# Optimization experiments

Measured on AMD Instinct MI355X. Metric: run time of the kernel, lower is better.

The kernel has to match this reference:

```python
import jax, jax.numpy as jnp
import numpy as np

DIM = 64
HEADS = 4

def setup_inputs() -> dict:
    key = jax.random.key(0)
    ks = jax.random.split(key, 8)
    b, c, h, w = 2, DIM, 64, 64
    x = jax.random.normal(ks[0], (b, c, h, w), dtype=jnp.float32)
    illu_feat = jax.random.normal(ks[1], (b, c, h, w), dtype=jnp.float32)
    s = 0.05
    qkv_w = jax.random.normal(ks[2], (3 * c, c), dtype=jnp.float32) * s
    qkv_b = jax.random.normal(ks[3], (3 * c,), dtype=jnp.float32) * s
    illu_w = jax.random.normal(ks[4], (c, c), dtype=jnp.float32) * s
    illu_b = jax.random.normal(ks[5], (c,), dtype=jnp.float32) * s
    proj_w = jax.random.normal(ks[6], (c, c), dtype=jnp.float32) * s
    proj_b = jax.random.normal(ks[7], (c,), dtype=jnp.float32) * s
    return {"x": x, "illu_feat": illu_feat, "qkv_w": qkv_w, "qkv_b": qkv_b,
            "illu_w": illu_w, "illu_b": illu_b, "proj_w": proj_w, "proj_b": proj_b}

def reference(x, illu_feat, qkv_w, qkv_b, illu_w, illu_b, proj_w, proj_b):
    b, c, h, w = x.shape
    heads = HEADS
    d = c // heads
    scale = float(d) ** -0.5
    hw = h * w
    # 1x1 convs are per-pixel matmuls over the channel dim
    xt = x.reshape(b, c, hw).transpose(0, 2, 1)            # [b, hw, c]
    qkv = xt @ qkv_w.T + qkv_b                              # [b, hw, 3c]
    # channel layout of qkv conv output is (three, heads, d)
    qkv = qkv.reshape(b, hw, 3, heads, d).transpose(2, 0, 3, 1, 4)  # [3, b, heads, hw, d]
    q, k, v = qkv[0], qkv[1], qkv[2]
    it = illu_feat.reshape(b, c, hw).transpose(0, 2, 1) @ illu_w.T + illu_b  # [b, hw, c]
    illu = it.reshape(b, hw, heads, d).transpose(0, 2, 1, 3)                 # [b, heads, hw, d]
    k = k + illu
    attn = jax.nn.softmax(jnp.einsum('bhnd,bhmd->bhnm', q, k) * scale, axis=-1)
    out = jnp.einsum('bhnm,bhmd->bhnd', attn, v)            # [b, heads, hw, d]
    out = out.transpose(0, 2, 1, 3).reshape(b, hw, c)       # channels = (heads, d)
    y = out @ proj_w.T + proj_b                             # [b, hw, c]
    return y.transpose(0, 2, 1).reshape(b, c, h, w)
```

## Files before the change

kernel.cpp:

```cpp
#include <hip/hip_runtime.h>
#include <hip/hip_bf16.h>
#include <math.h>

#define HW   4096
#define NC   64
#define NB   2
#define NHD  4
#define DH   16
#define NBH  (NB*NHD)

typedef __attribute__((ext_vector_type(4))) float f32x4;
typedef __attribute__((ext_vector_type(8))) short bf16x8;
typedef __attribute__((ext_vector_type(2))) unsigned int uint2v;

#define QSCALE 0.36067376022224087f

static __device__ __forceinline__ unsigned short bf16_bits(float f) {
    union { __hip_bfloat16 h; unsigned short u; } cv;
    cv.h = __float2bfloat16(f);
    return cv.u;
}
static __device__ __forceinline__ float bits_to_f(unsigned short b) {
    return __uint_as_float(((unsigned int)b) << 16);
}
static __device__ __forceinline__ unsigned int cvt_pk_bf16(float lo, float hi) {
    unsigned int r;
    asm("v_cvt_pk_bf16_f32 %0, %1, %2" : "=v"(r) : "v"(lo), "v"(hi));
    return r;
}

__global__ __launch_bounds__(256) void wprep_kernel(
    const float* __restrict__ qkv_w, const float* __restrict__ qkv_b,
    const float* __restrict__ illu_w, const float* __restrict__ illu_b,
    const float* __restrict__ proj_w,
    ushort* __restrict__ Wt, float* __restrict__ Bias, ushort* __restrict__ Wp)
{
    int idx = blockIdx.x * 256 + threadIdx.x;
    if (idx < 49152) {
        int k8 = idx & 15;
        int n  = (idx >> 4) & 15;
        int hl = (idx >> 8) & 1;
        int ct = (idx >> 9) & 7;
        int ot = idx >> 12;
        int c   = ct*16 + k8;
        int out = ot*16 + n;
        float w;
        if (ot < 4)       w = (c < 64) ? qkv_w[out*64 + c] * QSCALE : 0.f;
        else if (ot < 8)  w = (c < 64) ? qkv_w[out*64 + c]
                                       : illu_w[(out-64)*64 + (c-64)];
        else              w = (c < 64) ? qkv_w[out*64 + c] : 0.f;
        unsigned short hb = bf16_bits(w);
        Wt[idx] = (hl == 0) ? hb : bf16_bits(w - bits_to_f(hb));
    } else if (idx < 49344) {
        int out = idx - 49152;
        float bv = (out < 64)  ? qkv_b[out] * QSCALE
                 : (out < 128) ? qkv_b[out] + illu_b[out-64]
                 :               qkv_b[out];
        Bias[out] = bv;
    } else if (idx < 49344 + 8192) {
        int local = idx - 49344;
        int k8 = local & 15;
        int n  = (local >> 4) & 15;
        int hl = (local >> 8) & 1;
        int ct = (local >> 9) & 3;
        int ot = local >> 11;
        float w = proj_w[(ot*16 + n)*64 + ct*16 + k8];
        unsigned short hb = bf16_bits(w);
        Wp[local] = (hl == 0) ? hb : bf16_bits(w - bits_to_f(hb));
    }
}

__global__ __launch_bounds__(256) void qkv_kernel(
    const float* __restrict__ x, const float* __restrict__ illu,
    const ushort* __restrict__ Wt, const float* __restrict__ Bias,
    ushort* __restrict__ Qx, ushort* __restrict__ Kx, ushort* __restrict__ Vt)
{
    __shared__ alignas(16) float  xf[128*20];
    __shared__ alignas(16) ushort frag[8*16*32];

    int blk = blockIdx.x;
    int b   = blk & 1;
    int px0 = (blk >> 1) * 16;
    int tid = threadIdx.x;
    int w   = tid >> 6;
    int lane = tid & 63;
    int g   = lane >> 4;
    int n   = lane & 15;

    #pragma unroll
    for (int rep = 0; rep < 2; ++rep) {
        int id  = tid + rep*256;
        int row = id >> 2, seg = id & 3;
        const float* src = (row < 64) ? x    + (size_t)(b*NC + row)*HW
                                      : illu + (size_t)(b*NC + row - 64)*HW;
        float4 v = *(const float4*)(src + px0 + seg*4);
        *(float4*)(xf + row*20 + seg*4) = v;
    }
    __syncthreads();

    if (tid < 128) {
        int ct = tid >> 4, px = tid & 15;
        int swz = (px & 3) ^ ((px >> 2) & 3);
        union { ushort us[8]; bf16x8 v; } g0, g1, g2, g3;
        #pragma unroll
        for (int i = 0; i < 8; ++i) {
            float v  = xf[(ct*16 + i)*20 + px];
            unsigned short hb = bf16_bits(v);
            g0.us[i] = hb;
            g2.us[i] = bf16_bits(v - bits_to_f(hb));
            float v2 = xf[(ct*16 + 8 + i)*20 + px];
            unsigned short hb2 = bf16_bits(v2);
            g1.us[i] = hb2;
            g3.us[i] = bf16_bits(v2 - bits_to_f(hb2));
        }
        ushort* fb = frag + (ct*16 + px)*32;
        *(bf16x8*)(fb + ((0 ^ swz)*8)) = g0.v;
        *(bf16x8*)(fb + ((1 ^ swz)*8)) = g1.v;
        *(bf16x8*)(fb + ((2 ^ swz)*8)) = g2.v;
        *(bf16x8*)(fb + ((3 ^ swz)*8)) = g3.v;
    }
    __syncthreads();

    f32x4 zero4 = {0.f, 0.f, 0.f, 0.f};
    int px  = n;
    int swz = (px & 3) ^ ((px >> 2) & 3);
    const ushort* af_base = frag + px*32 + (g ^ swz)*8;

    #pragma unroll
    for (int j = 0; j < 3; ++j) {
        int ot  = w + 4*j;
        int nct = (ot >= 4 && ot < 8) ? 8 : 4;
        f32x4 acc = zero4;
        for (int ct = 0; ct < nct; ++ct) {
            bf16x8 af = *(const bf16x8*)(af_base + ct*512);
            const ushort* wb = Wt + ((size_t)(ot*8 + ct)*2)*256 + n*16 + (g&1)*8;
            bf16x8 bh = *(const bf16x8*)(wb);
            bf16x8 bl = *(const bf16x8*)(wb + 256);
            acc = __builtin_amdgcn_mfma_f32_16x16x32_bf16(af, bh, acc, 0, 0, 0);
            acc = __builtin_amdgcn_mfma_f32_16x16x32_bf16(af, bl, acc, 0, 0, 0);
        }
        float bias = Bias[ot*16 + n];
        float v0 = acc.x + bias, v1 = acc.y + bias;
        float v2 = acc.z + bias, v3 = acc.w + bias;
        if (ot < 8) {
            ushort* dst = (ot < 4) ? Qx : Kx;
            int head = ot & 3;
            size_t base = ((size_t)(b*NHD + head))*HW*32;
            #pragma unroll
            for (int r = 0; r < 4; ++r) {
                float val = (r==0? v0 : r==1? v1 : r==2? v2 : v3);
                int pxr = px0 + 4*g + r;
                unsigned short hb = bf16_bits(val);
                dst[base + (size_t)pxr*32 + n]      = hb;
                dst[base + (size_t)pxr*32 + 16 + n] = bf16_bits(val - bits_to_f(hb));
            }
        } else {
            int co = (ot - 8)*16 + n;
            uint2v pk;
            pk.x = cvt_pk_bf16(v0, v1);
            pk.y = cvt_pk_bf16(v2, v3);
            *(uint2v*)(Vt + ((size_t)(b*NC + co))*HW + px0 + 4*g) = pk;
        }
    }
}

#define KT   64
#define SPL  4
#define KPS  1024
#define NTS  (KPS/KT)

__global__ __launch_bounds__(512) void attn_kernel(
    const ushort* __restrict__ Qx, const ushort* __restrict__ Kx,
    const ushort* __restrict__ Vt, float* __restrict__ O)
{
    __shared__ alignas(16) ushort Ks[SPL][2][64*32];
    __shared__ alignas(16) ushort Vs[SPL][2][16*72];

    int blk  = blockIdx.x;
    int bh   = blk & 7;
    int q0   = (blk >> 3) * 64;
    int tid  = threadIdx.x;
    int w    = tid >> 6;
    int s    = w >> 1;
    int u    = w & 1;
    int lane = tid & 63;
    int g    = lane >> 4;
    int qc   = lane & 15;

    const ushort* Qb = Qx + (size_t)bh*HW*32;
    const ushort* Kb = Kx + (size_t)bh*HW*32 + (size_t)s*KPS*32;
    const ushort* Vb = Vt + (size_t)bh*DH*HW;

    int qrow0 = q0 + (u*2 + 0)*16 + qc;
    int qrow1 = q0 + (u*2 + 1)*16 + qc;
    bf16x8 qhi0 = *(const bf16x8*)(Qb + (size_t)qrow0*32 +      8*(g&1));
    bf16x8 qlo0 = *(const bf16x8*)(Qb + (size_t)qrow0*32 + 16 + 8*(g&1));
    bf16x8 qhi1 = *(const bf16x8*)(Qb + (size_t)qrow1*32 +      8*(g&1));
    bf16x8 qlo1 = *(const bf16x8*)(Qb + (size_t)qrow1*32 + 16 + 8*(g&1));

    f32x4 zero4 = {0.f, 0.f, 0.f, 0.f};
    f32x4 oacc0 = zero4, oacc1 = zero4;
    f32x4 lacc0 = zero4, lacc1 = zero4;

    int mconst = (qc & 3) ^ ((qc >> 2) & 3);
    const int koff = qc*32 + ((g ^ mconst)*8);
    const int voff = qc*72 + 4*g;

    int gt = tid & 127;
    int f0 = gt,        r0 = f0 >> 2, h0 = f0 & 3;
    int f1 = gt + 128,  r1 = f1 >> 2, h1 = f1 & 3;
    int s0 = (h0 ^ ((r0 & 3) ^ ((r0 >> 2) & 3))) * 8;
    int s1 = (h1 ^ ((r1 & 3) ^ ((r1 >> 2) & 3))) * 8;
    int vd = gt >> 3, vseg = gt & 7;

    {
        bf16x8 a0 = *(const bf16x8*)(Kb + (size_t)r0*32 + 8*h0);
        bf16x8 a1 = *(const bf16x8*)(Kb + (size_t)r1*32 + 8*h1);
        bf16x8 av = *(const bf16x8*)(Vb + (size_t)vd*HW + s*KPS + vseg*8);
        *(bf16x8*)(&Ks[s][0][0] + r0*32 + s0) = a0;
        *(bf16x8*)(&Ks[s][0][0] + r1*32 + s1) = a1;
        *(bf16x8*)(&Vs[s][0][0] + vd*72 + vseg*8) = av;
    }
    bf16x8 k0b = *(const bf16x8*)(Kb + (size_t)(KT + r0)*32 + 8*h0);
    bf16x8 k1b = *(const bf16x8*)(Kb + (size_t)(KT + r1)*32 + 8*h1);
    bf16x8 vb_ = *(const bf16x8*)(Vb + (size_t)vd*HW + s*KPS + KT + vseg*8);

    for (int t = 0; t < NTS; ++t) {
        __syncthreads();
        bf16x8 k0c = k0b, k1c = k1b, vc_ = vb_;
        if (t + 2 < NTS) {
            int kt = (t + 2) * KT;
            k0c = *(const bf16x8*)(Kb + (size_t)(kt + r0)*32 + 8*h0);
            k1c = *(const bf16x8*)(Kb + (size_t)(kt + r1)*32 + 8*h1);
            vc_ = *(const bf16x8*)(Vb + (size_t)vd*HW + s*KPS + kt + vseg*8);
        }

        const ushort* kr = &Ks[s][t & 1][0] + koff;
        const ushort* vr = &Vs[s][t & 1][0] + voff;
        unsigned int pe00 = 0, pe01 = 0, pe10 = 0, pe11 = 0;
        #pragma unroll
        for (int kb = 0; kb < 4; ++kb) {
            bf16x8 kfrag = *(const bf16x8*)(kr + kb*512);
            f32x4 sA = __builtin_amdgcn_mfma_f32_16x16x32_bf16(kfrag, qhi0, zero4, 0, 0, 0);
            sA = __builtin_amdgcn_mfma_f32_16x16x32_bf16(kfrag, qlo0, sA, 0, 0, 0);
            float a0 = __builtin_amdgcn_exp2f(sA.x);
            float a1 = __builtin_amdgcn_exp2f(sA.y);
            float a2 = __builtin_amdgcn_exp2f(sA.z);
            float a3 = __builtin_amdgcn_exp2f(sA.w);
            lacc0.x += a0; lacc0.y += a1; lacc0.z += a2; lacc0.w += a3;
            unsigned int alo = cvt_pk_bf16(a0, a1);
            unsigned int ahi = cvt_pk_bf16(a2, a3);
            f32x4 sB = __builtin_amdgcn_mfma_f32_16x16x32_bf16(kfrag, qhi1, zero4, 0, 0, 0);
            sB = __builtin_amdgcn_mfma_f32_16x16x32_bf16(kfrag, qlo1, sB, 0, 0, 0);
            float b0 = __builtin_amdgcn_exp2f(sB.x);
            float b1 = __builtin_amdgcn_exp2f(sB.y);
            float b2 = __builtin_amdgcn_exp2f(sB.z);
            float b3 = __builtin_amdgcn_exp2f(sB.w);
            lacc1.x += b0; lacc1.y += b1; lacc1.z += b2; lacc1.w += b3;
            unsigned int blo = cvt_pk_bf16(b0, b1);
            unsigned int bhi = cvt_pk_bf16(b2, b3);

            if ((kb & 1) == 0) { pe00 = alo; pe01 = ahi; pe10 = blo; pe11 = bhi; }
            else {
                uint2v vE = *(const uint2v*)(vr + (kb-1)*16);
                uint2v vO = *(const uint2v*)(vr + kb*16);
                union { unsigned int uu[4]; bf16x8 h; } pa, vv;
                vv.uu[0] = vE.x; vv.uu[1] = vE.y; vv.uu[2] = vO.x; vv.uu[3] = vO.y;
                pa.uu[0] = pe00; pa.uu[1] = pe01; pa.uu[2] = alo; pa.uu[3] = ahi;
                oacc0 = __builtin_amdgcn_mfma_f32_16x16x32_bf16(pa.h, vv.h, oacc0, 0, 0, 0);
                pa.uu[0] = pe10; pa.uu[1] = pe11; pa.uu[2] = blo; pa.uu[3] = bhi;
                oacc1 = __builtin_amdgcn_mfma_f32_16x16x32_bf16(pa.h, vv.h, oacc1, 0, 0, 0);
            }
        }

        if (t + 1 < NTS) {
            int nb = (t + 1) & 1;
            *(bf16x8*)(&Ks[s][nb][0] + r0*32 + s0) = k0b;
            *(bf16x8*)(&Ks[s][nb][0] + r1*32 + s1) = k1b;
            *(bf16x8*)(&Vs[s][nb][0] + vd*72 + vseg*8) = vb_;
            k0b = k0c; k1b = k1c; vb_ = vc_;
        }
    }

    float l0 = (lacc0.x + lacc0.y) + (lacc0.z + lacc0.w);
    l0 += __shfl_xor(l0, 16);
    l0 += __shfl_xor(l0, 32);
    float l1 = (lacc1.x + lacc1.y) + (lacc1.z + lacc1.w);
    l1 += __shfl_xor(l1, 16);
    l1 += __shfl_xor(l1, 32);

    __syncthreads();
    float* mrgF = (float*)&Ks[0][0][0];
    if (s > 0) {
        float* m0 = mrgF + (((((s-1)*2 + u)*2 + 0)*64 + lane)*5);
        m0[0] = oacc0.x; m0[1] = oacc0.y; m0[2] = oacc0.z; m0[3] = oacc0.w; m0[4] = l0;
        float* m1 = mrgF + (((((s-1)*2 + u)*2 + 1)*64 + lane)*5);
        m1[0] = oacc1.x; m1[1] = oacc1.y; m1[2] = oacc1.z; m1[3] = oacc1.w; m1[4] = l1;
    }
    __syncthreads();
    if (s == 0) {
        #pragma unroll
        for (int sp = 0; sp < 3; ++sp) {
            const float* m0 = mrgF + ((((sp*2 + u)*2 + 0)*64 + lane)*5);
            oacc0.x += m0[0]; oacc0.y += m0[1]; oacc0.z += m0[2]; oacc0.w += m0[3];
            l0 += m0[4];
            const float* m1 = mrgF + ((((sp*2 + u)*2 + 1)*64 + lane)*5);
            oacc1.x += m1[0]; oacc1.y += m1[1]; oacc1.z += m1[2]; oacc1.w += m1[3];
            l1 += m1[4];
        }
        int b = bh >> 2, h = bh & 3;
        float* Ob0 = O + ((size_t)b*HW + q0 + (u*2 + 0)*16)*NC + h*DH;
        float* Ob1 = O + ((size_t)b*HW + q0 + (u*2 + 1)*16)*NC + h*DH;
        #pragma unroll
        for (int r = 0; r < 4; ++r) {
            float lr0 = __shfl(l0, 4*g + r);
            float ov0 = (r==0? oacc0.x : r==1? oacc0.y : r==2? oacc0.z : oacc0.w);
            Ob0[(4*g + r)*NC + qc] = ov0 / lr0;
            float lr1 = __shfl(l1, 4*g + r);
            float ov1 = (r==0? oacc1.x : r==1? oacc1.y : r==2? oacc1.z : oacc1.w);
            Ob1[(4*g + r)*NC + qc] = ov1 / lr1;
        }
    }
}

__global__ __launch_bounds__(256) void proj_kernel(
    const float* __restrict__ O, const ushort* __restrict__ Wp,
    const float* __restrict__ proj_b, float* __restrict__ y)
{
    __shared__ alignas(16) float  of[64*20];
    __shared__ alignas(16) ushort frag[4*16*32];
    __shared__ alignas(16) float  ys[64][20];

    int blk = blockIdx.x;
    int b   = blk & 1;
    int px0 = (blk >> 1) * 16;
    int tid = threadIdx.x;
    int w   = tid >> 6;
    int lane = tid & 63;
    int g   = lane >> 4;
    int n   = lane & 15;

    {
        int px = tid >> 4, c4 = tid & 15;
        float4 v = *(const float4*)(O + ((size_t)(b*HW + px0 + px))*NC + c4*4);
        of[(c4*4+0)*20 + px] = v.x;
        of[(c4*4+1)*20 + px] = v.y;
        of[(c4*4+2)*20 + px] = v.z;
        of[(c4*4+3)*20 + px] = v.w;
    }
    __syncthreads();

    if (tid < 64) {
        int ct = tid >> 4, px = tid & 15;
        int swz = (px & 3) ^ ((px >> 2) & 3);
        union { ushort us[8]; bf16x8 v; } g0, g1, g2, g3;
        #pragma unroll
        for (int i = 0; i < 8; ++i) {
            float v  = of[(ct*16 + i)*20 + px];
            unsigned short hb = bf16_bits(v);
            g0.us[i] = hb;
            g2.us[i] = bf16_bits(v - bits_to_f(hb));
            float v2 = of[(ct*16 + 8 + i)*20 + px];
            unsigned short hb2 = bf16_bits(v2);
            g1.us[i] = hb2;
            g3.us[i] = bf16_bits(v2 - bits_to_f(hb2));
        }
        ushort* fb = frag + (ct*16 + px)*32;
        *(bf16x8*)(fb + ((0 ^ swz)*8)) = g0.v;
        *(bf16x8*)(fb + ((1 ^ swz)*8)) = g1.v;
        *(bf16x8*)(fb + ((2 ^ swz)*8)) = g2.v;
        *(bf16x8*)(fb + ((3 ^ swz)*8)) = g3.v;
    }
    __syncthreads();

    f32x4 acc = {0.f, 0.f, 0.f, 0.f};
    int px  = n;
    int swz = (px & 3) ^ ((px >> 2) & 3);
    const ushort* af_base = frag + px*32 + (g ^ swz)*8;
    #pragma unroll
    for (int ct = 0; ct < 4; ++ct) {
        bf16x8 af = *(const bf16x8*)(af_base + ct*512);
        const ushort* wb = Wp + ((size_t)(w*4 + ct)*2)*256 + n*16 + (g&1)*8;
        bf16x8 bh = *(const bf16x8*)(wb);
        bf16x8 bl = *(const bf16x8*)(wb + 256);
        acc = __builtin_amdgcn_mfma_f32_16x16x32_bf16(af, bh, acc, 0, 0, 0);
        acc = __builtin_amdgcn_mfma_f32_16x16x32_bf16(af, bl, acc, 0, 0, 0);
    }
    float bias = proj_b[w*16 + n];
    ys[w*16 + n][4*g+0] = acc.x + bias;
    ys[w*16 + n][4*g+1] = acc.y + bias;
    ys[w*16 + n][4*g+2] = acc.z + bias;
    ys[w*16 + n][4*g+3] = acc.w + bias;
    __syncthreads();

    {
        int row = tid >> 2, seg = tid & 3;
        float4 v;
        v.x = ys[row][seg*4+0]; v.y = ys[row][seg*4+1];
        v.z = ys[row][seg*4+2]; v.w = ys[row][seg*4+3];
        *(float4*)(y + ((size_t)(b*NC + row))*HW + px0 + seg*4) = v;
    }
}

extern "C" void kernel_launch(void* const* d_in, const int* in_sizes, int n_in,
                              void* d_out, int out_size, void* d_ws, size_t ws_size,
                              hipStream_t stream)
{
    const float* x      = (const float*)d_in[0];
    const float* illu   = (const float*)d_in[1];
    const float* qkv_w  = (const float*)d_in[2];
    const float* qkv_b  = (const float*)d_in[3];
    const float* illu_w = (const float*)d_in[4];
    const float* illu_b = (const float*)d_in[5];
    const float* proj_w = (const float*)d_in[6];
    const float* proj_b = (const float*)d_in[7];
    float* out = (float*)d_out;

    ushort* Qx   = (ushort*)d_ws;
    ushort* Kx   = Qx + (size_t)NBH*HW*32;
    ushort* Vt   = Kx + (size_t)NBH*HW*32;
    float*  O    = (float*)(Vt + (size_t)NBH*HW*DH);
    ushort* Wt   = (ushort*)(O + (size_t)NB*HW*NC);
    float*  Bias = (float*)(Wt + 49152);
    ushort* Wp   = (ushort*)(Bias + 192);

    hipLaunchKernelGGL(wprep_kernel, dim3(225), dim3(256), 0, stream,
                       qkv_w, qkv_b, illu_w, illu_b, proj_w, Wt, Bias, Wp);
    hipLaunchKernelGGL(qkv_kernel, dim3(512), dim3(256), 0, stream,
                       x, illu, Wt, Bias, Qx, Kx, Vt);
    hipLaunchKernelGGL(attn_kernel, dim3(512), dim3(512), 0, stream,
                       Qx, Kx, Vt, O);
    hipLaunchKernelGGL(proj_kernel, dim3(512), dim3(256), 0, stream,
                       O, Wp, proj_b, out);
}
```

Baseline: 48.18 us.

## Read V directly from global memory and compute softmax row sums via MFMA

Drops the LDS staging buffer for V: each lane now loads its V fragments straight from global memory, which removes the V shared-memory stores and the prefetch registers. The per-lane scalar accumulation of exp values, plus the shuffle reduction, is replaced by an extra MFMA against a ones vector, so the row sums come out in the same layout as the output accumulator. This frees VALU work and shared memory, but doubles the PV-stage MFMA count. V loads now go to global/L2 inside the inner loop with no prefetch, which may expose memory latency. Row sums are now taken from the bf16-rounded probabilities rather than the fp32 values.

```diff
diff --git a/kernel.cpp b/kernel.cpp
--- a/kernel.cpp
+++ b/kernel.cpp
@@ -174,7 +174,6 @@
     const ushort* __restrict__ Vt, float* __restrict__ O)
 {
     __shared__ alignas(16) ushort Ks[SPL][2][64*32];
-    __shared__ alignas(16) ushort Vs[SPL][2][16*72];
 
     int blk  = blockIdx.x;
     int bh   = blk & 7;
@@ -200,43 +199,42 @@
 
     f32x4 zero4 = {0.f, 0.f, 0.f, 0.f};
     f32x4 oacc0 = zero4, oacc1 = zero4;
-    f32x4 lacc0 = zero4, lacc1 = zero4;
+    f32x4 oaccL0 = zero4, oaccL1 = zero4;
+
+    union { unsigned int uu[4]; bf16x8 h; } ones;
+    ones.uu[0] = 0x3F803F80u; ones.uu[1] = 0x3F803F80u;
+    ones.uu[2] = 0x3F803F80u; ones.uu[3] = 0x3F803F80u;
 
     int mconst = (qc & 3) ^ ((qc >> 2) & 3);
     const int koff = qc*32 + ((g ^ mconst)*8);
-    const int voff = qc*72 + 4*g;
+    const ushort* vbase = Vb + (size_t)qc*HW + s*KPS + 4*g;
 
     int gt = tid & 127;
     int f0 = gt,        r0 = f0 >> 2, h0 = f0 & 3;
     int f1 = gt + 128,  r1 = f1 >> 2, h1 = f1 & 3;
     int s0 = (h0 ^ ((r0 & 3) ^ ((r0 >> 2) & 3))) * 8;
     int s1 = (h1 ^ ((r1 & 3) ^ ((r1 >> 2) & 3))) * 8;
-    int vd = gt >> 3, vseg = gt & 7;
 
     {
         bf16x8 a0 = *(const bf16x8*)(Kb + (size_t)r0*32 + 8*h0);
         bf16x8 a1 = *(const bf16x8*)(Kb + (size_t)r1*32 + 8*h1);
-        bf16x8 av = *(const bf16x8*)(Vb + (size_t)vd*HW + s*KPS + vseg*8);
         *(bf16x8*)(&Ks[s][0][0] + r0*32 + s0) = a0;
         *(bf16x8*)(&Ks[s][0][0] + r1*32 + s1) = a1;
-        *(bf16x8*)(&Vs[s][0][0] + vd*72 + vseg*8) = av;
     }
     bf16x8 k0b = *(const bf16x8*)(Kb + (size_t)(KT + r0)*32 + 8*h0);
     bf16x8 k1b = *(const bf16x8*)(Kb + (size_t)(KT + r1)*32 + 8*h1);
-    bf16x8 vb_ = *(const bf16x8*)(Vb + (size_t)vd*HW + s*KPS + KT + vseg*8);
 
     for (int t = 0; t < NTS; ++t) {
         __syncthreads();
-        bf16x8 k0c = k0b, k1c = k1b, vc_ = vb_;
+        bf16x8 k0c = k0b, k1c = k1b;
         if (t + 2 < NTS) {
             int kt = (t + 2) * KT;
             k0c = *(const bf16x8*)(Kb + (size_t)(kt + r0)*32 + 8*h0);
             k1c = *(const bf16x8*)(Kb + (size_t)(kt + r1)*32 + 8*h1);
-            vc_ = *(const bf16x8*)(Vb + (size_t)vd*HW + s*KPS + kt + vseg*8);
         }
 
         const ushort* kr = &Ks[s][t & 1][0] + koff;
-        const ushort* vr = &Vs[s][t & 1][0] + voff;
+        const ushort* vt = vbase + t*KT;
         unsigned int pe00 = 0, pe01 = 0, pe10 = 0, pe11 = 0;
         #pragma unroll
         for (int kb = 0; kb < 4; ++kb) {
@@ -247,7 +245,6 @@
             float a1 = __builtin_amdgcn_exp2f(sA.y);
             float a2 = __builtin_amdgcn_exp2f(sA.z);
             float a3 = __builtin_amdgcn_exp2f(sA.w);
-            lacc0.x += a0; lacc0.y += a1; lacc0.z += a2; lacc0.w += a3;
             unsigned int alo = cvt_pk_bf16(a0, a1);
             unsigned int ahi = cvt_pk_bf16(a2, a3);
             f32x4 sB = __builtin_amdgcn_mfma_f32_16x16x32_bf16(kfrag, qhi1, zero4, 0, 0, 0);
@@ -256,20 +253,21 @@
             float b1 = __builtin_amdgcn_exp2f(sB.y);
             float b2 = __builtin_amdgcn_exp2f(sB.z);
             float b3 = __builtin_amdgcn_exp2f(sB.w);
-            lacc1.x += b0; lacc1.y += b1; lacc1.z += b2; lacc1.w += b3;
             unsigned int blo = cvt_pk_bf16(b0, b1);
             unsigned int bhi = cvt_pk_bf16(b2, b3);
 
             if ((kb & 1) == 0) { pe00 = alo; pe01 = ahi; pe10 = blo; pe11 = bhi; }
             else {
-                uint2v vE = *(const uint2v*)(vr + (kb-1)*16);
-                uint2v vO = *(const uint2v*)(vr + kb*16);
+                uint2v vE = *(const uint2v*)(vt + (kb-1)*16);
+                uint2v vO = *(const uint2v*)(vt + kb*16);
                 union { unsigned int uu[4]; bf16x8 h; } pa, vv;
                 vv.uu[0] = vE.x; vv.uu[1] = vE.y; vv.uu[2] = vO.x; vv.uu[3] = vO.y;
                 pa.uu[0] = pe00; pa.uu[1] = pe01; pa.uu[2] = alo; pa.uu[3] = ahi;
-                oacc0 = __builtin_amdgcn_mfma_f32_16x16x32_bf16(pa.h, vv.h, oacc0, 0, 0, 0);
+                oacc0  = __builtin_amdgcn_mfma_f32_16x16x32_bf16(pa.h, vv.h,   oacc0,  0, 0, 0);
+                oaccL0 = __builtin_amdgcn_mfma_f32_16x16x32_bf16(pa.h, ones.h, oaccL0, 0, 0, 0);
                 pa.uu[0] = pe10; pa.uu[1] = pe11; pa.uu[2] = blo; pa.uu[3] = bhi;
-                oacc1 = __builtin_amdgcn_mfma_f32_16x16x32_bf16(pa.h, vv.h, oacc1, 0, 0, 0);
+                oacc1  = __builtin_amdgcn_mfma_f32_16x16x32_bf16(pa.h, vv.h,   oacc1,  0, 0, 0);
+                oaccL1 = __builtin_amdgcn_mfma_f32_16x16x32_bf16(pa.h, ones.h, oaccL1, 0, 0, 0);
             }
         }
 
@@ -277,48 +275,42 @@
             int nb = (t + 1) & 1;
             *(bf16x8*)(&Ks[s][nb][0] + r0*32 + s0) = k0b;
             *(bf16x8*)(&Ks[s][nb][0] + r1*32 + s1) = k1b;
-            *(bf16x8*)(&Vs[s][nb][0] + vd*72 + vseg*8) = vb_;
-            k0b = k0c; k1b = k1c; vb_ = vc_;
-        }
-    }
-
-    float l0 = (lacc0.x + lacc0.y) + (lacc0.z + lacc0.w);
-    l0 += __shfl_xor(l0, 16);
-    l0 += __shfl_xor(l0, 32);
-    float l1 = (lacc1.x + lacc1.y) + (lacc1.z + lacc1.w);
-    l1 += __shfl_xor(l1, 16);
-    l1 += __shfl_xor(l1, 32);
+            k0b = k0c; k1b = k1c;
+        }
+    }
 
     __syncthreads();
     float* mrgF = (float*)&Ks[0][0][0];
     if (s > 0) {
-        float* m0 = mrgF + (((((s-1)*2 + u)*2 + 0)*64 + lane)*5);
-        m0[0] = oacc0.x; m0[1] = oacc0.y; m0[2] = oacc0.z; m0[3] = oacc0.w; m0[4] = l0;
-        float* m1 = mrgF + (((((s-1)*2 + u)*2 + 1)*64 + lane)*5);
-        m1[0] = oacc1.x; m1[1] = oacc1.y; m1[2] = oacc1.z; m1[3] = oacc1.w; m1[4] = l1;
+        float* m0 = mrgF + (((((s-1)*2 + u)*2 + 0)*64 + lane)*8);
+        m0[0] = oacc0.x;  m0[1] = oacc0.y;  m0[2] = oacc0.z;  m0[3] = oacc0.w;
+        m0[4] = oaccL0.x; m0[5] = oaccL0.y; m0[6] = oaccL0.z; m0[7] = oaccL0.w;
+        float* m1 = mrgF + (((((s-1)*2 + u)*2 + 1)*64 + lane)*8);
+        m1[0] = oacc1.x;  m1[1] = oacc1.y;  m1[2] = oacc1.z;  m1[3] = oacc1.w;
+        m1[4] = oaccL1.x; m1[5] = oaccL1.y; m1[6] = oaccL1.z; m1[7] = oaccL1.w;
     }
     __syncthreads();
     if (s == 0) {
         #pragma unroll
         for (int sp = 0; sp < 3; ++sp) {
-            const float* m0 = mrgF + ((((sp*2 + u)*2 + 0)*64 + lane)*5);
-            oacc0.x += m0[0]; oacc0.y += m0[1]; oacc0.z += m0[2]; oacc0.w += m0[3];
-            l0 += m0[4];
-            const float* m1 = mrgF + ((((sp*2 + u)*2 + 1)*64 + lane)*5);
-            oacc1.x += m1[0]; oacc1.y += m1[1]; oacc1.z += m1[2]; oacc1.w += m1[3];
-            l1 += m1[4];
+            const float* m0 = mrgF + ((((sp*2 + u)*2 + 0)*64 + lane)*8);
+            oacc0.x  += m0[0]; oacc0.y  += m0[1]; oacc0.z  += m0[2]; oacc0.w  += m0[3];
+            oaccL0.x += m0[4]; oaccL0.y += m0[5]; oaccL0.z += m0[6]; oaccL0.w += m0[7];
+            const float* m1 = mrgF + ((((sp*2 + u)*2 + 1)*64 + lane)*8);
+            oacc1.x  += m1[0]; oacc1.y  += m1[1]; oacc1.z  += m1[2]; oacc1.w  += m1[3];
+            oaccL1.x += m1[4]; oaccL1.y += m1[5]; oaccL1.z += m1[6]; oaccL1.w += m1[7];
         }
         int b = bh >> 2, h = bh & 3;
         float* Ob0 = O + ((size_t)b*HW + q0 + (u*2 + 0)*16)*NC + h*DH;
         float* Ob1 = O + ((size_t)b*HW + q0 + (u*2 + 1)*16)*NC + h*DH;
         #pragma unroll
         for (int r = 0; r < 4; ++r) {
-            float lr0 = __shfl(l0, 4*g + r);
-            float ov0 = (r==0? oacc0.x : r==1? oacc0.y : r==2? oacc0.z : oacc0.w);
-            Ob0[(4*g + r)*NC + qc] = ov0 / lr0;
-            float lr1 = __shfl(l1, 4*g + r);
-            float ov1 = (r==0? oacc1.x : r==1? oacc1.y : r==2? oacc1.z : oacc1.w);
-            Ob1[(4*g + r)*NC + qc] = ov1 / lr1;
+            float ov0 = (r==0? oacc0.x  : r==1? oacc0.y  : r==2? oacc0.z  : oacc0.w);
+            float lv0 = (r==0? oaccL0.x : r==1? oaccL0.y : r==2? oaccL0.z : oaccL0.w);
+            Ob0[(4*g + r)*NC + qc] = ov0 / lv0;
+            float ov1 = (r==0? oacc1.x  : r==1? oacc1.y  : r==2? oacc1.z  : oacc1.w);
+            float lv1 = (r==0? oaccL1.x : r==1? oaccL1.y : r==2? oaccL1.z : oaccL1.w);
+            Ob1[(4*g + r)*NC + qc] = ov1 / lv1;
         }
     }
 }
```

After: 56.74 us. 17.8% more time.
